# Kernel optimization log

Hardware: AMD Instinct MI355X
Metric: run time of the kernel (lower is better)

## Reference

```python
import jax, jax.numpy as jnp
import numpy as np

P = 16          # patch_size
C = 3           # in_chans
D = 768         # embed_dim
V = 10240       # position_embedding_size
B, H, W = 16, 512, 512
N = (H // P) * (W // P)  # 1024 patches per image


def setup_inputs() -> dict:
    key = jax.random.key(0)
    k1, k2, k3, k4, k5 = jax.random.split(key, 5)
    pixel_values = jax.random.uniform(k1, (B, C, H, W), dtype=jnp.float32)
    position_ids = jax.random.randint(k2, (B, N, 2), 0, 32)  # (x, y) patch coords < pW/pH
    padding_positions = jax.random.randint(k3, (B, N), 0, 2).astype(jnp.bool_)
    w_proj = jax.random.normal(k4, (D, C * P * P), dtype=jnp.float32) * 0.02  # Linear weight (out, in)
    pos_table = jax.random.normal(k5, (2, V, D), dtype=jnp.float32) * 0.02
    return {
        "pixel_values": pixel_values,
        "w_proj": w_proj,
        "pos_table": pos_table,
        "position_ids": position_ids,
        "padding_positions": padding_positions,
    }


def reference(pixel_values, w_proj, pos_table, position_ids, padding_positions):
    b, c, h, w = pixel_values.shape
    ph, pw = h // P, w // P
    # Extract patches in Gemma4 C-P-P flatten order: (B, N, C*P*P)
    x = pixel_values.reshape(b, c, ph, P, pw, P)
    x = jnp.transpose(x, (0, 2, 4, 1, 3, 5)).reshape(b, ph * pw, c * P * P)
    patches = 2.0 * (x - 0.5)
    hidden = jnp.einsum('bnf,df->bnd', patches, w_proj)
    # Position embeddings: one_hot(ids) @ table summed over the 2 axes
    # == direct gather-add: table[0][x_id] + table[1][y_id]
    ids = jnp.clip(position_ids, 0)
    pos = pos_table[0][ids[..., 0]] + pos_table[1][ids[..., 1]]  # (B, N, D)
    pos = jnp.where(padding_positions[..., None], 0.0, pos)
    return hidden + pos
```

## Files before the change

kernel.cpp:

```cpp
#include <hip/hip_runtime.h>
#include <stdint.h>


typedef __attribute__((ext_vector_type(8))) short bfrag_t;
typedef __attribute__((ext_vector_type(4))) float f4_t;
typedef __attribute__((ext_vector_type(8))) unsigned short u16x8;
typedef __attribute__((ext_vector_type(4))) unsigned short u16x4;

#define M_TOT 16384
#define K_TOT 768
#define N_TOT 768
#define V_POS 10240
#define ROWS  40
#define KSTEP 5120

__device__ __forceinline__ unsigned short f2bf(float f) {
    unsigned int u = __float_as_uint(f);
    u += 0x7fffu + ((u >> 16) & 1u);
    return (unsigned short)(u >> 16);
}

__global__ __launch_bounds__(256) void wprep_kernel(
    const float* __restrict__ wp, const void* __restrict__ pad_in,
    unsigned short* __restrict__ Wb, unsigned char* __restrict__ mask)
{
    int bid = blockIdx.x, tid = threadIdx.x;
    if (bid < 288) {
        long idx = (long)bid * 256 + tid;
        const float4* s = (const float4*)(wp + (idx << 3));
        float4 v0 = s[0];
        float4 v1 = s[1];
        u16x8 o;
        o[0] = f2bf(v0.x); o[1] = f2bf(v0.y); o[2] = f2bf(v0.z); o[3] = f2bf(v0.w);
        o[4] = f2bf(v1.x); o[5] = f2bf(v1.y); o[6] = f2bf(v1.z); o[7] = f2bf(v1.w);
        *(u16x8*)(Wb + (idx << 3)) = o;
    } else {
        __shared__ int u8mode;
        if (tid == 0) u8mode = 0;
        __syncthreads();
        const unsigned int* pi = (const unsigned int*)pad_in;
        int local = 0;
        for (int i = tid; i < 4096; i += 256)
            if (pi[i] > 1u) local = 1;
        if (local) atomicOr(&u8mode, 1);
        __syncthreads();
        if (u8mode) {
            const unsigned char* p8 = (const unsigned char*)pad_in;
            for (int i = tid; i < M_TOT; i += 256) mask[i] = p8[i];
        } else {
            const int* p32 = (const int*)pad_in;
            for (int i = tid; i < M_TOT; i += 256) mask[i] = (unsigned char)(p32[i] != 0);
        }
    }
}

__global__ __launch_bounds__(256, 3) void fused_kernel(
    const float* __restrict__ px, const unsigned short* __restrict__ Bt,
    const int* __restrict__ pos_ids, const unsigned char* __restrict__ mask,
    const float* __restrict__ pos_table, float* __restrict__ out)
{
    __shared__ unsigned short As[2 * KSTEP];
    __shared__ unsigned short Bs[2 * KSTEP];

    const int tid  = threadIdx.x;
    const int wave = tid >> 6;
    const int lane = tid & 63;

    const int id   = blockIdx.x;
    const int xcd  = id & 7;
    const int slot = id >> 3;
    const int bmg  = slot / 6;
    const int bm   = xcd * 16 + bmg;
    const int bn   = slot - bmg * 6;
    const int m0   = bm << 7;
    const int n0   = bn << 7;
    const int bimg = bm >> 3;
    const int ph0  = (bm & 7) << 2;

    const int r16  = tid >> 4;
    const int ph_i = r16 >> 2;
    const int hlr  = r16 & 3;
    const int l16  = tid & 15;
    const int pw_b = l16 >> 2;
    const int pxo  = (l16 & 3) << 2;
    const int klA  = hlr * 16 + pxo;
    unsigned short* awr = As + (klA >> 5) * KSTEP + ((klA >> 3) & 3) * 8 + (klA & 7);
    const int rowb = ph_i * 32 + pw_b;

    const int nl  = tid >> 1;
    const int kst = tid & 1;
    const unsigned short* bgbase = Bt + (size_t)(n0 + nl) * K_TOT + kst * 32;
    unsigned short* bwr = Bs + kst * KSTEP + nl * ROWS;

    const int fr      = lane & 15;
    const int quad    = lane >> 4;
    const int row_off = (wave & 1) << 6;
    const int col_off = (wave >> 1) << 6;
    const unsigned short* ards = As + (size_t)(row_off + fr) * ROWS + quad * 8;
    const unsigned short* brds = Bs + (size_t)(col_off + fr) * ROWS + quad * 8;

    float4 P[8];
    u16x8  Q[4];
    {
        const float* prow = px + (((size_t)bimg * 3 + 0) * 512
                                  + (size_t)(ph0 + ph_i) * 16 + hlr) * 512 + (l16 << 2);
#pragma unroll
        for (int j = 0; j < 8; ++j) P[j] = *(const float4*)(prow + (j << 6));
#pragma unroll
        for (int u = 0; u < 4; ++u) Q[u] = *(const u16x8*)(bgbase + (u << 3));
    }

    f4_t acc[4][4] = {};

    for (int kk = 0; kk < 12; ++kk) {
#pragma unroll
        for (int j = 0; j < 8; ++j) {
            u16x4 v;
            v[0] = f2bf(2.f * P[j].x - 1.f);
            v[1] = f2bf(2.f * P[j].y - 1.f);
            v[2] = f2bf(2.f * P[j].z - 1.f);
            v[3] = f2bf(2.f * P[j].w - 1.f);
            *(u16x4*)(awr + (rowb + 4 * j) * ROWS) = v;
        }
#pragma unroll
        for (int u = 0; u < 4; ++u)
            *(u16x8*)(bwr + (u << 3)) = Q[u];
        __syncthreads();

        if (kk < 11) {
            const int k2 = kk + 1;
            const int c  = k2 >> 2;
            const int hl = ((k2 & 3) << 2) + hlr;
            const float* prow = px + (((size_t)bimg * 3 + c) * 512
                                      + (size_t)(ph0 + ph_i) * 16 + hl) * 512 + (l16 << 2);
#pragma unroll
            for (int j = 0; j < 8; ++j) P[j] = *(const float4*)(prow + (j << 6));
            const unsigned short* bg = bgbase + k2 * 64;
#pragma unroll
            for (int u = 0; u < 4; ++u) Q[u] = *(const u16x8*)(bg + (u << 3));
        }

#pragma unroll
        for (int ks = 0; ks < 2; ++ks) {
            bfrag_t a[4], b[4];
#pragma unroll
            for (int i = 0; i < 4; ++i)
                a[i] = *(const bfrag_t*)(ards + ks * KSTEP + i * 16 * ROWS);
#pragma unroll
            for (int i = 0; i < 4; ++i)
                b[i] = *(const bfrag_t*)(brds + ks * KSTEP + i * 16 * ROWS);
#pragma unroll
            for (int mi = 0; mi < 4; ++mi)
#pragma unroll
                for (int ni = 0; ni < 4; ++ni)
                    acc[mi][ni] = __builtin_amdgcn_mfma_f32_16x16x32_bf16(
                        a[mi], b[ni], acc[mi][ni], 0, 0, 0);
        }
        __syncthreads();
    }

#pragma unroll
    for (int mi = 0; mi < 4; ++mi) {
#pragma unroll
        for (int reg = 0; reg < 4; ++reg) {
            int gm  = m0 + row_off + mi * 16 + (quad << 2) + reg;
            int xid = pos_ids[2 * gm];
            int yid = pos_ids[2 * gm + 1];
            xid = xid < 0 ? 0 : xid;
            yid = yid < 0 ? 0 : yid;
            bool p = mask[gm] != 0;
            const float* t0 = pos_table + (size_t)xid * N_TOT + n0 + col_off;
            const float* t1 = pos_table + (size_t)(V_POS + yid) * N_TOT + n0 + col_off;
            float* orow = out + (size_t)gm * N_TOT + n0 + col_off;
#pragma unroll
            for (int ni = 0; ni < 4; ++ni) {
                int cc = ni * 16 + fr;
                float pos = p ? 0.f : (t0[cc] + t1[cc]);
                orow[cc] = acc[mi][ni][reg] + pos;
            }
        }
    }
}

extern "C" void kernel_launch(void* const* d_in, const int* in_sizes, int n_in,
                              void* d_out, int out_size, void* d_ws, size_t ws_size,
                              hipStream_t stream) {
    const float* px  = (const float*)d_in[0];
    const float* wp  = (const float*)d_in[1];
    const float* pt  = (const float*)d_in[2];
    const int*   pid = (const int*)d_in[3];
    const void*  pad = d_in[4];

    unsigned short* Wb   = (unsigned short*)d_ws;
    unsigned char*  maskp = (unsigned char*)(Wb + (size_t)N_TOT * K_TOT);

    wprep_kernel<<<289, 256, 0, stream>>>(wp, pad, Wb, maskp);
    fused_kernel<<<768, 256, 0, stream>>>(px, Wb, pid, maskp, pt, (float*)d_out);
}
```

Measured before the change: 182.5 us.

## Fuse weight bf16 conversion and padding detection into single pipelined GEMM kernel

Removes the separate prep kernel: the fused kernel now reads fp32 weights directly and converts them to bf16 while staging into LDS, and each wave detects the padding mask format inline. The K loop is restructured into 24 steps of 32 with register double-buffering two tiles ahead and a single LDS-wait barrier per step. This saves a kernel launch and the workspace round trip, but every block repeats the weight conversion and reads twice the weight bytes. Occupancy hint drops from 3 to 2 blocks per CU.

Result: faster. 177.3 us (-2.8%).

```diff
diff --git a/kernel.cpp b/kernel.cpp
--- a/kernel.cpp
+++ b/kernel.cpp
@@ -4,15 +4,11 @@
 
 typedef __attribute__((ext_vector_type(8))) short bfrag_t;
 typedef __attribute__((ext_vector_type(4))) float f4_t;
-typedef __attribute__((ext_vector_type(8))) unsigned short u16x8;
 typedef __attribute__((ext_vector_type(4))) unsigned short u16x4;
 
-#define M_TOT 16384
-#define K_TOT 768
-#define N_TOT 768
 #define V_POS 10240
-#define ROWS  40
-#define KSTEP 5120
+#define RS 40
+#define ABUF 5120
 
 __device__ __forceinline__ unsigned short f2bf(float f) {
     unsigned int u = __float_as_uint(f);
@@ -20,47 +16,17 @@
     return (unsigned short)(u >> 16);
 }
 
-__global__ __launch_bounds__(256) void wprep_kernel(
-    const float* __restrict__ wp, const void* __restrict__ pad_in,
-    unsigned short* __restrict__ Wb, unsigned char* __restrict__ mask)
-{
-    int bid = blockIdx.x, tid = threadIdx.x;
-    if (bid < 288) {
-        long idx = (long)bid * 256 + tid;
-        const float4* s = (const float4*)(wp + (idx << 3));
-        float4 v0 = s[0];
-        float4 v1 = s[1];
-        u16x8 o;
-        o[0] = f2bf(v0.x); o[1] = f2bf(v0.y); o[2] = f2bf(v0.z); o[3] = f2bf(v0.w);
-        o[4] = f2bf(v1.x); o[5] = f2bf(v1.y); o[6] = f2bf(v1.z); o[7] = f2bf(v1.w);
-        *(u16x8*)(Wb + (idx << 3)) = o;
-    } else {
-        __shared__ int u8mode;
-        if (tid == 0) u8mode = 0;
-        __syncthreads();
-        const unsigned int* pi = (const unsigned int*)pad_in;
-        int local = 0;
-        for (int i = tid; i < 4096; i += 256)
-            if (pi[i] > 1u) local = 1;
-        if (local) atomicOr(&u8mode, 1);
-        __syncthreads();
-        if (u8mode) {
-            const unsigned char* p8 = (const unsigned char*)pad_in;
-            for (int i = tid; i < M_TOT; i += 256) mask[i] = p8[i];
-        } else {
-            const int* p32 = (const int*)pad_in;
-            for (int i = tid; i < M_TOT; i += 256) mask[i] = (unsigned char)(p32[i] != 0);
-        }
-    }
+__device__ __forceinline__ void lgkm_barrier() {
+    __builtin_amdgcn_s_waitcnt(0xC07F);
+    __builtin_amdgcn_s_barrier();
 }
 
-__global__ __launch_bounds__(256, 3) void fused_kernel(
-    const float* __restrict__ px, const unsigned short* __restrict__ Bt,
-    const int* __restrict__ pos_ids, const unsigned char* __restrict__ mask,
+__global__ __launch_bounds__(256, 2) void fused_kernel(
+    const float* __restrict__ px, const float* __restrict__ wp,
+    const int* __restrict__ pos_ids, const unsigned int* __restrict__ pad_in,
     const float* __restrict__ pos_table, float* __restrict__ out)
 {
-    __shared__ unsigned short As[2 * KSTEP];
-    __shared__ unsigned short Bs[2 * KSTEP];
+    __shared__ unsigned short LDS[4 * ABUF];
 
     const int tid  = threadIdx.x;
     const int wave = tid >> 6;
@@ -77,88 +43,95 @@
     const int bimg = bm >> 3;
     const int ph0  = (bm & 7) << 2;
 
-    const int r16  = tid >> 4;
-    const int ph_i = r16 >> 2;
-    const int hlr  = r16 & 3;
-    const int l16  = tid & 15;
-    const int pw_b = l16 >> 2;
-    const int pxo  = (l16 & 3) << 2;
-    const int klA  = hlr * 16 + pxo;
-    unsigned short* awr = As + (klA >> 5) * KSTEP + ((klA >> 3) & 3) * 8 + (klA & 7);
-    const int rowb = ph_i * 32 + pw_b;
+    const bool u8mode = __any(pad_in[lane] > 1u);
 
-    const int nl  = tid >> 1;
-    const int kst = tid & 1;
-    const unsigned short* bgbase = Bt + (size_t)(n0 + nl) * K_TOT + kst * 32;
-    unsigned short* bwr = Bs + kst * KSTEP + nl * ROWS;
+    int aw[4], bw[4], bgb[4];
+#pragma unroll
+    for (int j = 0; j < 4; ++j) {
+        int f4A = j * 64 + lane;
+        int kh  = f4A >> 7;
+        int f4i = f4A & 127;
+        int pw  = f4i >> 2;
+        int e   = f4i & 3;
+        aw[j] = (wave * 32 + pw) * RS + kh * 16 + e * 4;
+        int offb = j * 1024 + lane * 16;
+        int colL = offb >> 7;
+        int win  = offb & 127;
+        bgb[j] = colL * 3072 + win;
+        bw[j]  = (wave * 32 + colL) * RS + (win >> 2);
+    }
+    const float* abase = px + (((size_t)bimg * 3) * 512 + (size_t)(ph0 + wave) * 16) * 512;
+    const char*  bbase = (const char*)(wp + (size_t)(n0 + wave * 32) * 768);
+    const int    aglo  = lane * 4;
+
+    float4 FA[2][4], FB[2][4];
+
+    auto load_tile = [&](int t) {
+        int s = t & 1;
+        const float* ab = abase + (t >> 3) * 262144 + ((t * 2) & 15) * 512;
+#pragma unroll
+        for (int j = 0; j < 4; ++j)
+            FA[s][j] = *(const float4*)(ab + j * 256 + aglo);
+        const char* bb = bbase + t * 128;
+#pragma unroll
+        for (int j = 0; j < 4; ++j)
+            FB[s][j] = *(const float4*)(bb + bgb[j]);
+    };
+    auto store_tile = [&](int t) {
+        int s = t & 1;
+        unsigned short* A = LDS + s * ABUF;
+        unsigned short* B = LDS + 2 * ABUF + s * ABUF;
+#pragma unroll
+        for (int j = 0; j < 4; ++j) {
+            u16x4 v;
+            v[0] = f2bf(2.f * FA[s][j].x - 1.f);
+            v[1] = f2bf(2.f * FA[s][j].y - 1.f);
+            v[2] = f2bf(2.f * FA[s][j].z - 1.f);
+            v[3] = f2bf(2.f * FA[s][j].w - 1.f);
+            *(u16x4*)(A + aw[j]) = v;
+            u16x4 w;
+            w[0] = f2bf(FB[s][j].x);
+            w[1] = f2bf(FB[s][j].y);
+            w[2] = f2bf(FB[s][j].z);
+            w[3] = f2bf(FB[s][j].w);
+            *(u16x4*)(B + bw[j]) = w;
+        }
+    };
 
     const int fr      = lane & 15;
     const int quad    = lane >> 4;
     const int row_off = (wave & 1) << 6;
     const int col_off = (wave >> 1) << 6;
-    const unsigned short* ards = As + (size_t)(row_off + fr) * ROWS + quad * 8;
-    const unsigned short* brds = Bs + (size_t)(col_off + fr) * ROWS + quad * 8;
-
-    float4 P[8];
-    u16x8  Q[4];
-    {
-        const float* prow = px + (((size_t)bimg * 3 + 0) * 512
-                                  + (size_t)(ph0 + ph_i) * 16 + hlr) * 512 + (l16 << 2);
-#pragma unroll
-        for (int j = 0; j < 8; ++j) P[j] = *(const float4*)(prow + (j << 6));
-#pragma unroll
-        for (int u = 0; u < 4; ++u) Q[u] = *(const u16x8*)(bgbase + (u << 3));
-    }
 
     f4_t acc[4][4] = {};
 
-    for (int kk = 0; kk < 12; ++kk) {
-#pragma unroll
-        for (int j = 0; j < 8; ++j) {
-            u16x4 v;
-            v[0] = f2bf(2.f * P[j].x - 1.f);
-            v[1] = f2bf(2.f * P[j].y - 1.f);
-            v[2] = f2bf(2.f * P[j].z - 1.f);
-            v[3] = f2bf(2.f * P[j].w - 1.f);
-            *(u16x4*)(awr + (rowb + 4 * j) * ROWS) = v;
-        }
-#pragma unroll
-        for (int u = 0; u < 4; ++u)
-            *(u16x8*)(bwr + (u << 3)) = Q[u];
-        __syncthreads();
-
-        if (kk < 11) {
-            const int k2 = kk + 1;
-            const int c  = k2 >> 2;
-            const int hl = ((k2 & 3) << 2) + hlr;
-            const float* prow = px + (((size_t)bimg * 3 + c) * 512
-                                      + (size_t)(ph0 + ph_i) * 16 + hl) * 512 + (l16 << 2);
-#pragma unroll
-            for (int j = 0; j < 8; ++j) P[j] = *(const float4*)(prow + (j << 6));
-            const unsigned short* bg = bgbase + k2 * 64;
-#pragma unroll
-            for (int u = 0; u < 4; ++u) Q[u] = *(const u16x8*)(bg + (u << 3));
-        }
+    load_tile(0);
+    load_tile(1);
+    store_tile(0);
+    lgkm_barrier();
 
 #pragma unroll
-        for (int ks = 0; ks < 2; ++ks) {
-            bfrag_t a[4], b[4];
+    for (int kk = 0; kk < 24; ++kk) {
+        if (kk < 22) load_tile(kk + 2);
+        if (kk < 23) store_tile(kk + 1);
+        const unsigned short* Ab = LDS + (kk & 1) * ABUF + (row_off + fr) * RS + quad * 8;
+        const unsigned short* Bb = LDS + 2 * ABUF + (kk & 1) * ABUF + (col_off + fr) * RS + quad * 8;
+        bfrag_t a[4], b[4];
 #pragma unroll
-            for (int i = 0; i < 4; ++i)
-                a[i] = *(const bfrag_t*)(ards + ks * KSTEP + i * 16 * ROWS);
+        for (int i = 0; i < 4; ++i) a[i] = *(const bfrag_t*)(Ab + i * 16 * RS);
 #pragma unroll
-            for (int i = 0; i < 4; ++i)
-                b[i] = *(const bfrag_t*)(brds + ks * KSTEP + i * 16 * ROWS);
+        for (int i = 0; i < 4; ++i) b[i] = *(const bfrag_t*)(Bb + i * 16 * RS);
 #pragma unroll
-            for (int mi = 0; mi < 4; ++mi)
+        for (int mi = 0; mi < 4; ++mi)
 #pragma unroll
-                for (int ni = 0; ni < 4; ++ni)
-                    acc[mi][ni] = __builtin_amdgcn_mfma_f32_16x16x32_bf16(
-                        a[mi], b[ni], acc[mi][ni], 0, 0, 0);
-        }
-        __syncthreads();
+            for (int ni = 0; ni < 4; ++ni)
+                acc[mi][ni] = __builtin_amdgcn_mfma_f32_16x16x32_bf16(
+                    a[mi], b[ni], acc[mi][ni], 0, 0, 0);
+        if (kk < 23) lgkm_barrier();
     }
 
+    const unsigned char* pad8 = (const unsigned char*)pad_in;
+    const int colbase = n0 + col_off;
 #pragma unroll
     for (int mi = 0; mi < 4; ++mi) {
 #pragma unroll
@@ -168,10 +141,10 @@
             int yid = pos_ids[2 * gm + 1];
             xid = xid < 0 ? 0 : xid;
             yid = yid < 0 ? 0 : yid;
-            bool p = mask[gm] != 0;
-            const float* t0 = pos_table + (size_t)xid * N_TOT + n0 + col_off;
-            const float* t1 = pos_table + (size_t)(V_POS + yid) * N_TOT + n0 + col_off;
-            float* orow = out + (size_t)gm * N_TOT + n0 + col_off;
+            bool p = u8mode ? (pad8[gm] != 0) : (pad_in[gm] != 0u);
+            const float* t0 = pos_table + (size_t)xid * 768 + colbase;
+            const float* t1 = pos_table + (size_t)(V_POS + yid) * 768 + colbase;
+            float* orow = out + (size_t)gm * 768 + colbase;
 #pragma unroll
             for (int ni = 0; ni < 4; ++ni) {
                 int cc = ni * 16 + fr;
@@ -185,15 +158,11 @@
 extern "C" void kernel_launch(void* const* d_in, const int* in_sizes, int n_in,
                               void* d_out, int out_size, void* d_ws, size_t ws_size,
                               hipStream_t stream) {
-    const float* px  = (const float*)d_in[0];
-    const float* wp  = (const float*)d_in[1];
-    const float* pt  = (const float*)d_in[2];
-    const int*   pid = (const int*)d_in[3];
-    const void*  pad = d_in[4];
+    const float*        px  = (const float*)d_in[0];
+    const float*        wp  = (const float*)d_in[1];
+    const float*        pt  = (const float*)d_in[2];
+    const int*          pid = (const int*)d_in[3];
+    const unsigned int* pad = (const unsigned int*)d_in[4];
 
-    unsigned short* Wb   = (unsigned short*)d_ws;
-    unsigned char*  maskp = (unsigned char*)(Wb + (size_t)N_TOT * K_TOT);
-
-    wprep_kernel<<<289, 256, 0, stream>>>(wp, pad, Wb, maskp);
-    fused_kernel<<<768, 256, 0, stream>>>(px, Wb, pid, maskp, pt, (float*)d_out);
+    fused_kernel<<<768, 256, 0, stream>>>(px, wp, pid, pad, pt, (float*)d_out);
 }
```
